# Performance work log

Hardware: AMD Instinct MI355X
Metric: run time of the kernel (lower is better)

The kernel has to match this reference:

```python
import jax, jax.numpy as jnp
import numpy as np

GRID_SIZE = 16
SPLINE_ORDER = 4
GRID_LO, GRID_HI = -1.0, 1.0
NUM_GRID = 2 * SPLINE_ORDER + GRID_SIZE + 1  # 25 knots
NUM_COEFFS = GRID_SIZE + SPLINE_ORDER        # 20 basis functions
B, IN_F, OUT_F = 2048, 512, 512


def _make_grid():
    h = (GRID_HI - GRID_LO) / GRID_SIZE
    t1 = -SPLINE_ORDER * h + GRID_LO
    t2 = (GRID_SIZE + SPLINE_ORDER + 1) * h + GRID_LO
    return jnp.linspace(t1, t2, NUM_GRID)


def _bspline_basis(x, grid):
    # x: [..., in]; returns [..., in, NUM_COEFFS] via De Boor recursion
    xe = x[..., None]
    bases = ((xe >= grid[:-1]) & (xe < grid[1:])).astype(x.dtype)
    for k in range(1, SPLINE_ORDER + 1):
        left = (xe - grid[:-k - 1]) / (grid[k:-1] - grid[:-k - 1]) * bases[..., :-1]
        right = (grid[k + 1:] - xe) / (grid[k + 1:] - grid[1:-k]) * bases[..., 1:]
        bases = left + right
    return bases


def setup_inputs() -> dict:
    key = jax.random.key(0)
    ks = jax.random.split(key, 5)
    fan = np.sqrt(1.0 / IN_F)
    return {
        "x": jax.random.normal(ks[0], (B, IN_F), jnp.float32),
        "prelu_weight": jax.random.normal(ks[1], (OUT_F, IN_F), jnp.float32) * 0.25,
        "base_weight": jax.random.uniform(ks[2], (OUT_F, IN_F), jnp.float32, -fan, fan),
        "spline_weight": jax.random.uniform(ks[3], (OUT_F, IN_F), jnp.float32, -fan, fan),
        "spline_coeffs": jax.random.normal(ks[4], (OUT_F, IN_F, NUM_COEFFS), jnp.float32) * 0.1,
    }


def reference(x, prelu_weight, base_weight, spline_weight, spline_coeffs):
    grid = _make_grid()
    xc = jnp.clip(x, GRID_LO, GRID_HI)
    pos = jax.nn.relu(xc)
    neg = xc - pos
    # base path: sum_j base_w[i,j]*(prelu_w[i,j]*neg[b,j] + pos[b,j])
    # fused: never materialize the [out, B, in] prelu output
    base = neg @ (base_weight * prelu_weight).T + pos @ base_weight.T  # [B, out]
    basis = _bspline_basis(xc, grid)  # [B, in, K]
    # spline path: fold spline_weight into coeffs, single contraction over (j,k)
    eff_coeffs = spline_weight[:, :, None] * spline_coeffs  # [out, in, K]
    spline = jnp.einsum('bjk,ijk->bi', basis, eff_coeffs)   # [B, out]
    return base + spline
```

## Files before the change

### kernel.cpp

```cpp
#include <hip/hip_runtime.h>


typedef _Float16 half_t;
typedef __attribute__((ext_vector_type(8))) _Float16 half8;
typedef __attribute__((ext_vector_type(4))) float floatx4;

#define B_DIM   2048
#define J_DIM   512
#define O_DIM   512
#define SLOTS   22
#define K_TOT   (J_DIM * SLOTS)
#define MTILE   128
#define NTILE   128
#define BK      32
#define KSPLIT_P 8
#define KSPLIT_A 11
#define ZERO_BLKS 64

__device__ __forceinline__ void bspline5(float xc, int& k0, float Nv[5]) {
    const float invS = 7.68f;
    float u = (xc + 1.5f) * invS;
    int m = (int)u;
    m = min(max(m, 3), 19);
    k0 = m - 4;
    Nv[0] = 1.f; Nv[1] = 0.f; Nv[2] = 0.f; Nv[3] = 0.f; Nv[4] = 0.f;
#pragma unroll
    for (int d = 1; d <= 4; ++d) {
        float nw[5];
        float inv_d = 1.0f / (float)d;
#pragma unroll
        for (int r = 0; r < 5; ++r) {
            if (r > d) { nw[r] = 0.f; continue; }
            float kk = (float)(m - d + r);
            float acc = 0.f;
            if (r >= 1) acc += (u - kk) * Nv[r - 1];
            if (r < d)  acc += (kk + (float)(d + 1) - u) * Nv[r];
            nw[r] = acc * inv_d;
        }
#pragma unroll
        for (int r = 0; r < 5; ++r) Nv[r] = nw[r];
    }
}

__global__ __launch_bounds__(256) void prep_all(const float* __restrict__ x,
                                                const float* __restrict__ pw,
                                                const float* __restrict__ bw,
                                                const float* __restrict__ sw,
                                                const float* __restrict__ sc,
                                                half_t* __restrict__ A,
                                                half_t* __restrict__ Ct,
                                                float* __restrict__ out) {
    __shared__ half_t rec[J_DIM * SLOTS];
    int bid = blockIdx.x;
    int t = threadIdx.x;

    if (bid < ZERO_BLKS) {
        float4* o = (float4*)out;
        int base = bid * 4096;
#pragma unroll
        for (int i = 0; i < 16; ++i)
            o[base + i * 256 + t] = make_float4(0.f, 0.f, 0.f, 0.f);
        return;
    }

    if (bid < ZERO_BLKS + O_DIM) {
        int i = bid - ZERO_BLKS;
#pragma unroll
        for (int jj = 0; jj < 2; ++jj) {
            int j = t + jj * 256;
            size_t ij = (size_t)i * J_DIM + j;
            float s = sw[ij], b = bw[ij], p = pw[ij];
            const float4* scp4 = (const float4*)(sc + ij * 20);
            half_t* r = rec + j * SLOTS;
#pragma unroll
            for (int v = 0; v < 5; ++v) {
                float4 c4 = scp4[v];
                r[v * 4 + 0] = (half_t)(s * c4.x);
                r[v * 4 + 1] = (half_t)(s * c4.y);
                r[v * 4 + 2] = (half_t)(s * c4.z);
                r[v * 4 + 3] = (half_t)(s * c4.w);
            }
            r[20] = (half_t)(b * p);
            r[21] = (half_t)b;
        }
        __syncthreads();
        const uint4* src = (const uint4*)rec;
        uint4* dst = (uint4*)(Ct + (size_t)i * K_TOT);
        for (int idx = t; idx < (J_DIM * SLOTS * 2) / 16; idx += 256) dst[idx] = src[idx];
        return;
    }

    int b = bid - ZERO_BLKS - O_DIM;
#pragma unroll
    for (int jj = 0; jj < 2; ++jj) {
        int j = t + jj * 256;
        float xv = x[(size_t)b * J_DIM + j];
        float xc = fminf(fmaxf(xv, -1.f), 1.f);
        float pos = fmaxf(xc, 0.f);
        float neg = xc - pos;
        int k0; float Nv[5];
        bspline5(xc, k0, Nv);
        half_t* r = rec + j * SLOTS;
#pragma unroll
        for (int k = 0; k < 20; ++k) r[k] = (half_t)0.f;
#pragma unroll
        for (int rr = 0; rr < 5; ++rr) {
            int k = k0 + rr;
            if (k >= 0) r[k] = (half_t)Nv[rr];
        }
        r[20] = (half_t)neg;
        r[21] = (half_t)pos;
    }
    __syncthreads();
    const uint4* src = (const uint4*)rec;
    uint4* dst = (uint4*)(A + (size_t)b * K_TOT);
    for (int i = t; i < (J_DIM * SLOTS * 2) / 16; i += 256) dst[i] = src[i];
}

template<int KSPLIT_T, int OUTMODE>
__global__ __launch_bounds__(256, 3) void gemm_f16(const half_t* __restrict__ A,
                                                   const half_t* __restrict__ Bt,
                                                   float* __restrict__ out) {
    constexpr int KS_LEN_T = K_TOT / KSPLIT_T;
    constexpr int KCH_T = KS_LEN_T / BK;
    static_assert(KS_LEN_T % BK == 0, "k-split must be BK-aligned");
    static_assert(KCH_T >= 2, "pipeline needs >= 2 chunks");

    __shared__ half_t As[3][MTILE * BK];
    __shared__ half_t Bs[3][NTILE * BK];

    int m0 = blockIdx.x * MTILE;
    int n0 = blockIdx.y * NTILE;
    int ks = blockIdx.z * KS_LEN_T;

    int t = threadIdx.x;
    int w = t >> 6;
    int l = t & 63;
    int wm = w >> 1, wn = w & 1;

    floatx4 acc[4][4] = {};

    int lrow = l >> 2;
    int lkof = (((l & 3) ^ ((l >> 3) & 3)) * 8);

    const half_t* gA = A + (size_t)m0 * K_TOT + ks;
    const half_t* gB = Bt + (size_t)n0 * K_TOT + ks;

    int q = l >> 4;
    int fr = l & 15;
    int qs = (q ^ ((fr >> 1) & 3)) * 8;

#define ISSUE_LOADS(c, p)                                                     \
    {                                                                         \
        int kb = (c) * BK;                                                    \
        _Pragma("unroll")                                                     \
        for (int n = 0; n < 2; ++n) {                                         \
            int r = (w * 2 + n) * 16 + lrow;                                  \
            __builtin_amdgcn_global_load_lds(                                 \
                (const __attribute__((address_space(1))) unsigned int*)       \
                    (gA + (size_t)r * K_TOT + kb + lkof),                     \
                (__attribute__((address_space(3))) unsigned int*)             \
                    (&As[p][0] + (w * 2 + n) * 512),                          \
                16, 0, 0);                                                    \
            __builtin_amdgcn_global_load_lds(                                 \
                (const __attribute__((address_space(1))) unsigned int*)       \
                    (gB + (size_t)r * K_TOT + kb + lkof),                     \
                (__attribute__((address_space(3))) unsigned int*)             \
                    (&Bs[p][0] + (w * 2 + n) * 512),                          \
                16, 0, 0);                                                    \
        }                                                                     \
    }

    ISSUE_LOADS(0, 0)
    ISSUE_LOADS(1, 1)

    int pb = 0;
    for (int c = 0; c < KCH_T; ++c) {
        if (c + 2 < KCH_T) {
            asm volatile("s_waitcnt vmcnt(4)" ::: "memory");
            __builtin_amdgcn_s_barrier();
            int pn = pb + 2; if (pn >= 3) pn -= 3;
            ISSUE_LOADS(c + 2, pn)
        } else if (c + 2 == KCH_T) {
            asm volatile("s_waitcnt vmcnt(4)" ::: "memory");
            __builtin_amdgcn_s_barrier();
        } else {
            asm volatile("s_waitcnt vmcnt(0)" ::: "memory");
            __builtin_amdgcn_s_barrier();
        }

        half8 af[4], bf[4];
#pragma unroll
        for (int mt = 0; mt < 4; ++mt)
            af[mt] = *(const half8*)(&As[pb][0] + (wm * 64 + mt * 16 + fr) * BK + qs);
#pragma unroll
        for (int nt = 0; nt < 4; ++nt)
            bf[nt] = *(const half8*)(&Bs[pb][0] + (wn * 64 + nt * 16 + fr) * BK + qs);

        __builtin_amdgcn_s_setprio(1);
#pragma unroll
        for (int mt = 0; mt < 4; ++mt)
#pragma unroll
            for (int nt = 0; nt < 4; ++nt)
                acc[mt][nt] = __builtin_amdgcn_mfma_f32_16x16x32_f16(
                    af[mt], bf[nt], acc[mt][nt], 0, 0, 0);
        __builtin_amdgcn_s_setprio(0);

        if (++pb == 3) pb = 0;
    }
#undef ISSUE_LOADS

    if (OUTMODE == 0) {
        float* dst = out + (size_t)blockIdx.z * ((size_t)B_DIM * O_DIM);
#pragma unroll
        for (int mt = 0; mt < 4; ++mt)
#pragma unroll
            for (int nt = 0; nt < 4; ++nt) {
                int rr = m0 + wm * 64 + mt * 16 + q * 4;
                int cc = n0 + wn * 64 + nt * 16 + fr;
#pragma unroll
                for (int r = 0; r < 4; ++r)
                    dst[(size_t)(rr + r) * O_DIM + cc] = acc[mt][nt][r];
            }
    } else {
#pragma unroll
        for (int mt = 0; mt < 4; ++mt)
#pragma unroll
            for (int nt = 0; nt < 4; ++nt) {
                int rr = m0 + wm * 64 + mt * 16 + q * 4;
                int cc = n0 + wn * 64 + nt * 16 + fr;
#pragma unroll
                for (int r = 0; r < 4; ++r)
                    atomicAdd(out + (size_t)(rr + r) * O_DIM + cc, acc[mt][nt][r]);
            }
    }
}

__global__ __launch_bounds__(256) void reduce8(const float* __restrict__ parts,
                                               float* __restrict__ out) {
    constexpr int N4 = B_DIM * O_DIM / 4;
    int i = blockIdx.x * 256 + threadIdx.x;
    const float4* p = (const float4*)parts;
    float4 a = p[i];
#pragma unroll
    for (int z = 1; z < KSPLIT_P; ++z) {
        float4 b = p[(size_t)z * N4 + i];
        a.x += b.x; a.y += b.y; a.z += b.z; a.w += b.w;
    }
    ((float4*)out)[i] = a;
}

__global__ __launch_bounds__(256) void kan_fallback(const float* __restrict__ x,
                                                    const float* __restrict__ pw,
                                                    const float* __restrict__ bw,
                                                    const float* __restrict__ sw,
                                                    const float* __restrict__ sc,
                                                    float* __restrict__ out) {
    __shared__ float s_neg[J_DIM], s_pos[J_DIM], s_bas[J_DIM][5];
    __shared__ int s_k0[J_DIM];
    int b = blockIdx.x;
    int t = threadIdx.x;
#pragma unroll
    for (int jj = 0; jj < 2; ++jj) {
        int j = t + jj * 256;
        float xv = x[(size_t)b * J_DIM + j];
        float xc = fminf(fmaxf(xv, -1.f), 1.f);
        float pos = fmaxf(xc, 0.f);
        s_pos[j] = pos;
        s_neg[j] = xc - pos;
        int k0; float Nv[5];
        bspline5(xc, k0, Nv);
        s_k0[j] = k0;
#pragma unroll
        for (int r = 0; r < 5; ++r) s_bas[j][r] = Nv[r];
    }
    __syncthreads();
    for (int i = t; i < O_DIM; i += 256) {
        float acc = 0.f;
        for (int j = 0; j < J_DIM; ++j) {
            size_t ij = (size_t)i * J_DIM + j;
            float bwv = bw[ij];
            acc += bwv * (pw[ij] * s_neg[j] + s_pos[j]);
            int k0 = s_k0[j];
            const float* cp = sc + ij * 20;
            float sp = 0.f;
#pragma unroll
            for (int r = 0; r < 5; ++r) {
                int k = k0 + r;
                if (k >= 0) sp += s_bas[j][r] * cp[k];
            }
            acc += sw[ij] * sp;
        }
        out[(size_t)b * O_DIM + i] = acc;
    }
}

extern "C" void kernel_launch(void* const* d_in, const int* in_sizes, int n_in,
                              void* d_out, int out_size, void* d_ws, size_t ws_size,
                              hipStream_t stream) {
    const float* x  = (const float*)d_in[0];
    const float* pw = (const float*)d_in[1];
    const float* bw = (const float*)d_in[2];
    const float* sw = (const float*)d_in[3];
    const float* sc = (const float*)d_in[4];
    float* out = (float*)d_out;

    const size_t abct = (size_t)(B_DIM + O_DIM) * K_TOT * sizeof(half_t);
    const size_t parts_bytes = (size_t)KSPLIT_P * B_DIM * O_DIM * sizeof(float);

    if (ws_size >= abct + parts_bytes) {
        half_t* A  = (half_t*)d_ws;
        half_t* Ct = A + (size_t)B_DIM * K_TOT;
        float* parts = (float*)((char*)d_ws + abct);

        prep_all<<<ZERO_BLKS + O_DIM + B_DIM, 256, 0, stream>>>(x, pw, bw, sw, sc, A, Ct, out);
        dim3 g(B_DIM / MTILE, O_DIM / NTILE, KSPLIT_P);
        gemm_f16<KSPLIT_P, 0><<<g, 256, 0, stream>>>(A, Ct, parts);
        reduce8<<<(B_DIM * O_DIM / 4) / 256, 256, 0, stream>>>(parts, out);
    } else if (ws_size >= abct) {
        half_t* A  = (half_t*)d_ws;
        half_t* Ct = A + (size_t)B_DIM * K_TOT;

        prep_all<<<ZERO_BLKS + O_DIM + B_DIM, 256, 0, stream>>>(x, pw, bw, sw, sc, A, Ct, out);
        dim3 g(B_DIM / MTILE, O_DIM / NTILE, KSPLIT_A);
        gemm_f16<KSPLIT_A, 1><<<g, 256, 0, stream>>>(A, Ct, out);
    } else {
        kan_fallback<<<B_DIM, 256, 0, stream>>>(x, pw, bw, sw, sc, out);
    }
}
```

Baseline: 128.0 us.

## Rework prep kernel with vectorized packed stores and remap GEMM block order

The prep kernel is split into two roles. Weight rows now go straight from registers to global memory as packed half2 words written with 16-byte stores, with no shared-memory staging. The activation path handles two batch rows per block using float4 loads and a single 16-byte copy out. The GEMM remaps its linear block id so that the eight k-split blocks of one output tile are scheduled next to each other, which aims at better cache locality. The output-zeroing blocks and the atomic-add path for small workspaces are removed, and small workspaces now fall back to the scalar kernel.

```diff
diff --git a/kernel.cpp b/kernel.cpp
--- a/kernel.cpp
+++ b/kernel.cpp
@@ -13,9 +13,7 @@
 #define MTILE   128
 #define NTILE   128
 #define BK      32
-#define KSPLIT_P 8
-#define KSPLIT_A 11
-#define ZERO_BLKS 64
+#define KSPLIT  8
 
 __device__ __forceinline__ void bspline5(float xc, int& k0, float Nv[5]) {
     const float invS = 7.68f;
@@ -42,96 +40,108 @@
     }
 }
 
-__global__ __launch_bounds__(256) void prep_all(const float* __restrict__ x,
-                                                const float* __restrict__ pw,
-                                                const float* __restrict__ bw,
-                                                const float* __restrict__ sw,
-                                                const float* __restrict__ sc,
-                                                half_t* __restrict__ A,
-                                                half_t* __restrict__ Ct,
-                                                float* __restrict__ out) {
-    __shared__ half_t rec[J_DIM * SLOTS];
+__device__ __forceinline__ unsigned packh2(float a, float b) {
+    half_t ha = (half_t)a, hb = (half_t)b;
+    unsigned short ua = __builtin_bit_cast(unsigned short, ha);
+    unsigned short ub = __builtin_bit_cast(unsigned short, hb);
+    return (unsigned)ua | ((unsigned)ub << 16);
+}
+
+__global__ __launch_bounds__(256) void prep2(const float* __restrict__ x,
+                                             const float* __restrict__ pw,
+                                             const float* __restrict__ bw,
+                                             const float* __restrict__ sw,
+                                             const float* __restrict__ sc,
+                                             half_t* __restrict__ A,
+                                             half_t* __restrict__ Ct) {
+    __shared__ half_t sbuf[2][128 * 88];
     int bid = blockIdx.x;
     int t = threadIdx.x;
-
-    if (bid < ZERO_BLKS) {
-        float4* o = (float4*)out;
-        int base = bid * 4096;
-#pragma unroll
-        for (int i = 0; i < 16; ++i)
-            o[base + i * 256 + t] = make_float4(0.f, 0.f, 0.f, 0.f);
+    int sub = t >> 7;
+    int jq  = t & 127;
+    int j0  = jq * 4;
+
+    if (bid < 256) {
+        int i = bid * 2 + sub;
+        size_t ij0 = (size_t)i * J_DIM + j0;
+        float4 s4 = *(const float4*)(sw + ij0);
+        float4 b4 = *(const float4*)(bw + ij0);
+        float4 p4 = *(const float4*)(pw + ij0);
+        const float4* sp4 = (const float4*)(sc + ij0 * 20);
+        unsigned u[44];
+#pragma unroll
+        for (int jj = 0; jj < 4; ++jj) {
+            float s = ((const float*)&s4)[jj];
+            float b = ((const float*)&b4)[jj];
+            float p = ((const float*)&p4)[jj];
+#pragma unroll
+            for (int v = 0; v < 5; ++v) {
+                float4 c4 = sp4[jj * 5 + v];
+                u[jj * 11 + v * 2 + 0] = packh2(s * c4.x, s * c4.y);
+                u[jj * 11 + v * 2 + 1] = packh2(s * c4.z, s * c4.w);
+            }
+            u[jj * 11 + 10] = packh2(b * p, b);
+        }
+        uint4* dst = (uint4*)(Ct + (size_t)i * K_TOT + (size_t)j0 * SLOTS);
+#pragma unroll
+        for (int v = 0; v < 11; ++v)
+            dst[v] = make_uint4(u[4 * v], u[4 * v + 1], u[4 * v + 2], u[4 * v + 3]);
         return;
     }
 
-    if (bid < ZERO_BLKS + O_DIM) {
-        int i = bid - ZERO_BLKS;
-#pragma unroll
-        for (int jj = 0; jj < 2; ++jj) {
-            int j = t + jj * 256;
-            size_t ij = (size_t)i * J_DIM + j;
-            float s = sw[ij], b = bw[ij], p = pw[ij];
-            const float4* scp4 = (const float4*)(sc + ij * 20);
-            half_t* r = rec + j * SLOTS;
-#pragma unroll
-            for (int v = 0; v < 5; ++v) {
-                float4 c4 = scp4[v];
-                r[v * 4 + 0] = (half_t)(s * c4.x);
-                r[v * 4 + 1] = (half_t)(s * c4.y);
-                r[v * 4 + 2] = (half_t)(s * c4.z);
-                r[v * 4 + 3] = (half_t)(s * c4.w);
-            }
-            r[20] = (half_t)(b * p);
-            r[21] = (half_t)b;
-        }
-        __syncthreads();
-        const uint4* src = (const uint4*)rec;
-        uint4* dst = (uint4*)(Ct + (size_t)i * K_TOT);
-        for (int idx = t; idx < (J_DIM * SLOTS * 2) / 16; idx += 256) dst[idx] = src[idx];
-        return;
-    }
-
-    int b = bid - ZERO_BLKS - O_DIM;
-#pragma unroll
-    for (int jj = 0; jj < 2; ++jj) {
-        int j = t + jj * 256;
-        float xv = x[(size_t)b * J_DIM + j];
+    int b0 = (bid - 256) * 2;
+    int b = b0 + sub;
+    float4 x4 = *(const float4*)(x + (size_t)b * J_DIM + j0);
+    half_t* reg = &sbuf[sub][jq * 88];
+
+    half8 z;
+#pragma unroll
+    for (int e = 0; e < 8; ++e) z[e] = (half_t)0.f;
+#pragma unroll
+    for (int v = 0; v < 11; ++v) *(half8*)(reg + v * 8) = z;
+
+#pragma unroll
+    for (int jj = 0; jj < 4; ++jj) {
+        float xv = ((const float*)&x4)[jj];
         float xc = fminf(fmaxf(xv, -1.f), 1.f);
         float pos = fmaxf(xc, 0.f);
         float neg = xc - pos;
         int k0; float Nv[5];
         bspline5(xc, k0, Nv);
-        half_t* r = rec + j * SLOTS;
-#pragma unroll
-        for (int k = 0; k < 20; ++k) r[k] = (half_t)0.f;
+        half_t* rb = reg + jj * SLOTS;
 #pragma unroll
         for (int rr = 0; rr < 5; ++rr) {
             int k = k0 + rr;
-            if (k >= 0) r[k] = (half_t)Nv[rr];
-        }
-        r[20] = (half_t)neg;
-        r[21] = (half_t)pos;
+            if (k >= 0) rb[k] = (half_t)Nv[rr];
+        }
+        *(unsigned*)(rb + 20) = packh2(neg, pos);
     }
     __syncthreads();
-    const uint4* src = (const uint4*)rec;
-    uint4* dst = (uint4*)(A + (size_t)b * K_TOT);
-    for (int i = t; i < (J_DIM * SLOTS * 2) / 16; i += 256) dst[i] = src[i];
-}
-
-template<int KSPLIT_T, int OUTMODE>
+
+    const uint4* src = (const uint4*)&sbuf[0][0];
+    uint4* dst = (uint4*)(A + (size_t)b0 * K_TOT);
+#pragma unroll
+    for (int v = 0; v < 11; ++v) dst[v * 256 + t] = src[v * 256 + t];
+}
+
 __global__ __launch_bounds__(256, 3) void gemm_f16(const half_t* __restrict__ A,
                                                    const half_t* __restrict__ Bt,
                                                    float* __restrict__ out) {
-    constexpr int KS_LEN_T = K_TOT / KSPLIT_T;
-    constexpr int KCH_T = KS_LEN_T / BK;
-    static_assert(KS_LEN_T % BK == 0, "k-split must be BK-aligned");
-    static_assert(KCH_T >= 2, "pipeline needs >= 2 chunks");
+    constexpr int KS_LEN = K_TOT / KSPLIT;
+    constexpr int KCH = KS_LEN / BK;
 
     __shared__ half_t As[3][MTILE * BK];
     __shared__ half_t Bs[3][NTILE * BK];
 
-    int m0 = blockIdx.x * MTILE;
-    int n0 = blockIdx.y * NTILE;
-    int ks = blockIdx.z * KS_LEN_T;
+    int lid = blockIdx.x + (B_DIM / MTILE) * (blockIdx.y + (O_DIM / NTILE) * blockIdx.z);
+    int bz = lid & 7;
+    int rem = lid >> 3;
+    int bx = rem & (B_DIM / MTILE - 1);
+    int by = rem >> 4;
+
+    int m0 = bx * MTILE;
+    int n0 = by * NTILE;
+    int ks = bz * KS_LEN;
 
     int t = threadIdx.x;
     int w = t >> 6;
@@ -175,13 +185,13 @@
     ISSUE_LOADS(1, 1)
 
     int pb = 0;
-    for (int c = 0; c < KCH_T; ++c) {
-        if (c + 2 < KCH_T) {
+    for (int c = 0; c < KCH; ++c) {
+        if (c + 2 < KCH) {
             asm volatile("s_waitcnt vmcnt(4)" ::: "memory");
             __builtin_amdgcn_s_barrier();
             int pn = pb + 2; if (pn >= 3) pn -= 3;
             ISSUE_LOADS(c + 2, pn)
-        } else if (c + 2 == KCH_T) {
+        } else if (c + 2 == KCH) {
             asm volatile("s_waitcnt vmcnt(4)" ::: "memory");
             __builtin_amdgcn_s_barrier();
         } else {
@@ -210,30 +220,17 @@
     }
 #undef ISSUE_LOADS
 
-    if (OUTMODE == 0) {
-        float* dst = out + (size_t)blockIdx.z * ((size_t)B_DIM * O_DIM);
-#pragma unroll
-        for (int mt = 0; mt < 4; ++mt)
-#pragma unroll
-            for (int nt = 0; nt < 4; ++nt) {
-                int rr = m0 + wm * 64 + mt * 16 + q * 4;
-                int cc = n0 + wn * 64 + nt * 16 + fr;
-#pragma unroll
-                for (int r = 0; r < 4; ++r)
-                    dst[(size_t)(rr + r) * O_DIM + cc] = acc[mt][nt][r];
-            }
-    } else {
-#pragma unroll
-        for (int mt = 0; mt < 4; ++mt)
-#pragma unroll
-            for (int nt = 0; nt < 4; ++nt) {
-                int rr = m0 + wm * 64 + mt * 16 + q * 4;
-                int cc = n0 + wn * 64 + nt * 16 + fr;
-#pragma unroll
-                for (int r = 0; r < 4; ++r)
-                    atomicAdd(out + (size_t)(rr + r) * O_DIM + cc, acc[mt][nt][r]);
-            }
-    }
+    float* dst = out + (size_t)bz * ((size_t)B_DIM * O_DIM);
+#pragma unroll
+    for (int mt = 0; mt < 4; ++mt)
+#pragma unroll
+        for (int nt = 0; nt < 4; ++nt) {
+            int rr = m0 + wm * 64 + mt * 16 + q * 4;
+            int cc = n0 + wn * 64 + nt * 16 + fr;
+#pragma unroll
+            for (int r = 0; r < 4; ++r)
+                dst[(size_t)(rr + r) * O_DIM + cc] = acc[mt][nt][r];
+        }
 }
 
 __global__ __launch_bounds__(256) void reduce8(const float* __restrict__ parts,
@@ -243,7 +240,7 @@
     const float4* p = (const float4*)parts;
     float4 a = p[i];
 #pragma unroll
-    for (int z = 1; z < KSPLIT_P; ++z) {
+    for (int z = 1; z < KSPLIT; ++z) {
         float4 b = p[(size_t)z * N4 + i];
         a.x += b.x; a.y += b.y; a.z += b.z; a.w += b.w;
     }
@@ -306,24 +303,17 @@
     float* out = (float*)d_out;
 
     const size_t abct = (size_t)(B_DIM + O_DIM) * K_TOT * sizeof(half_t);
-    const size_t parts_bytes = (size_t)KSPLIT_P * B_DIM * O_DIM * sizeof(float);
+    const size_t parts_bytes = (size_t)KSPLIT * B_DIM * O_DIM * sizeof(float);
 
     if (ws_size >= abct + parts_bytes) {
         half_t* A  = (half_t*)d_ws;
         half_t* Ct = A + (size_t)B_DIM * K_TOT;
         float* parts = (float*)((char*)d_ws + abct);
 
-        prep_all<<<ZERO_BLKS + O_DIM + B_DIM, 256, 0, stream>>>(x, pw, bw, sw, sc, A, Ct, out);
-        dim3 g(B_DIM / MTILE, O_DIM / NTILE, KSPLIT_P);
-        gemm_f16<KSPLIT_P, 0><<<g, 256, 0, stream>>>(A, Ct, parts);
+        prep2<<<256 + B_DIM / 2, 256, 0, stream>>>(x, pw, bw, sw, sc, A, Ct);
+        dim3 g(B_DIM / MTILE, O_DIM / NTILE, KSPLIT);
+        gemm_f16<<<g, 256, 0, stream>>>(A, Ct, parts);
         reduce8<<<(B_DIM * O_DIM / 4) / 256, 256, 0, stream>>>(parts, out);
-    } else if (ws_size >= abct) {
-        half_t* A  = (half_t*)d_ws;
-        half_t* Ct = A + (size_t)B_DIM * K_TOT;
-
-        prep_all<<<ZERO_BLKS + O_DIM + B_DIM, 256, 0, stream>>>(x, pw, bw, sw, sc, A, Ct, out);
-        dim3 g(B_DIM / MTILE, O_DIM / NTILE, KSPLIT_A);
-        gemm_f16<KSPLIT_A, 1><<<g, 256, 0, stream>>>(A, Ct, out);
     } else {
         kan_fallback<<<B_DIM, 256, 0, stream>>>(x, pw, bw, sw, sc, out);
     }
```

New measurement: 129.2 us. No clear change (+1.0%).
